# Kernel tuning notes

Hardware: AMD Instinct MI355X
Metric: run time of the kernel (lower is better)

## Reference

```python
import jax, jax.numpy as jnp
import numpy as np

LN_EPS = 1e-5

def _layernorm(x, gamma, beta):
    mu = jnp.mean(x, axis=-1, keepdims=True)
    var = jnp.mean(jnp.square(x - mu), axis=-1, keepdims=True)
    return (x - mu) * jax.lax.rsqrt(var + LN_EPS) * gamma + beta

def _gcn_layer(A_hat, H, W, b, g, beta):
    # batched dense-equivalent of per-batch torch.sparse.mm: (B,N,N)@(B,N,F)
    H = jnp.einsum('bnm,bmf->bnf', A_hat, H)
    H = H @ W + b            # Linear
    H = _layernorm(H, g, beta)
    return jax.nn.relu(H)    # dropout is identity in eval

def setup_inputs() -> dict:
    key = jax.random.key(0)
    ks = jax.random.split(key, 8)
    B, N, F, Hd, K, G = 16, 2048, 64, 256, 128, 18
    fuse = Hd + G  # 274
    return {
        'A_hat': jax.random.uniform(ks[0], (B, N, N), dtype=jnp.float32),
        'X': jax.random.normal(ks[1], (B, N, F), dtype=jnp.float32),
        'global_vec': jax.random.normal(ks[2], (B, G), dtype=jnp.float32),
        'W1': jax.random.normal(ks[3], (F, Hd), dtype=jnp.float32) / np.sqrt(F),
        'b1': jnp.zeros((Hd,), jnp.float32),
        'g1': jnp.ones((Hd,), jnp.float32),
        'beta1': jnp.zeros((Hd,), jnp.float32),
        'W2': jax.random.normal(ks[4], (Hd, Hd), dtype=jnp.float32) / np.sqrt(Hd),
        'b2': jnp.zeros((Hd,), jnp.float32),
        'g2': jnp.ones((Hd,), jnp.float32),
        'beta2': jnp.zeros((Hd,), jnp.float32),
        'Ws': jax.random.normal(ks[5], (fuse, 1), dtype=jnp.float32) / np.sqrt(fuse),
        'bs': jnp.zeros((1,), jnp.float32),
        'Wa': jax.random.normal(ks[6], (fuse, K), dtype=jnp.float32) / np.sqrt(fuse),
        'ba': jnp.zeros((K,), jnp.float32),
    }

def reference(A_hat, X, global_vec, W1, b1, g1, beta1, W2, b2, g2, beta2, Ws, bs, Wa, ba):
    H = _gcn_layer(A_hat, X, W1, b1, g1, beta1)
    H = _gcn_layer(A_hat, H, W2, b2, g2, beta2)
    gcnout = jnp.mean(H, axis=1)                       # 'mean' readout -> (B, hidden)
    fused = jnp.concatenate([gcnout, global_vec], axis=-1)  # (B, hidden+18)
    pred_y_reg = (fused @ Ws + bs)[:, 0]               # (B,)
    pred_arr_reg = fused @ Wa + ba                     # (B, K)
    return pred_y_reg, pred_arr_reg
```

## Files before the change

kernel.cpp:

```cpp
#include <hip/hip_runtime.h>

typedef unsigned short u16;
typedef __attribute__((ext_vector_type(8))) short bf16x8;
typedef __attribute__((ext_vector_type(16))) float f32x16;

__device__ __forceinline__ unsigned f2bf(float f) {
  unsigned u = __float_as_uint(f);
  return (u + 0x7fffu + ((u >> 16) & 1u)) >> 16;
}

__device__ __forceinline__ void async16(const u16* g, u16* l) {
  __builtin_amdgcn_global_load_lds(
      (const __attribute__((address_space(1))) void*)g,
      (__attribute__((address_space(3))) void*)l, 16, 0, 0);
}

__global__ __launch_bounds__(256) void prep(
    const float* __restrict__ A, u16* __restrict__ Abf,
    const float* __restrict__ X, u16* __restrict__ Xbf,
    const float* __restrict__ W1, u16* __restrict__ W1T,
    const float* __restrict__ W2, u16* __restrict__ W2T,
    float* __restrict__ GCN)
{
  const long long gid = (long long)blockIdx.x * 256 + threadIdx.x;
  const long long stride = (long long)gridDim.x * 256;
  for (long long i = gid; i < 8388608LL; i += stride) {
    const float4 a = ((const float4*)A)[2 * i];
    const float4 b = ((const float4*)A)[2 * i + 1];
    uint4 r;
    r.x = f2bf(a.x) | (f2bf(a.y) << 16);
    r.y = f2bf(a.z) | (f2bf(a.w) << 16);
    r.z = f2bf(b.x) | (f2bf(b.y) << 16);
    r.w = f2bf(b.z) | (f2bf(b.w) << 16);
    ((uint4*)Abf)[i] = r;
  }
  for (long long i = gid; i < 262144LL; i += stride) {
    const float4 a = ((const float4*)X)[2 * i];
    const float4 b = ((const float4*)X)[2 * i + 1];
    uint4 r;
    r.x = f2bf(a.x) | (f2bf(a.y) << 16);
    r.y = f2bf(a.z) | (f2bf(a.w) << 16);
    r.z = f2bf(b.x) | (f2bf(b.y) << 16);
    r.w = f2bf(b.z) | (f2bf(b.w) << 16);
    ((uint4*)Xbf)[i] = r;
  }
  for (long long i = gid; i < 16384LL; i += stride) {
    const int c = (int)(i >> 6), r = (int)(i & 63);
    W1T[i] = (u16)f2bf(W1[r * 256 + c]);
  }
  for (long long i = gid; i < 65536LL; i += stride) {
    const int c = (int)(i >> 8), r = (int)(i & 255);
    W2T[i] = (u16)f2bf(W2[r * 256 + c]);
  }
  if (gid < 4096) GCN[gid] = 0.f;
}

template<int EPI>
__global__ __launch_bounds__(512, 2) void mm128(
    const u16* __restrict__ Aop, const u16* __restrict__ Bop,
    int K, int lda, int ldb, int ldc,
    long long sA, long long sB, long long sC,
    const float* __restrict__ bias, const float* __restrict__ gam,
    const float* __restrict__ bet, u16* __restrict__ Cb, float* __restrict__ gcn)
{
  __shared__ __align__(16) u16 As[2][128 * 64];
  __shared__ __align__(16) u16 Bs[2][256 * 64];
  const int tid = threadIdx.x;
  const int w = tid >> 6, lane = tid & 63, l31 = lane & 31, half = lane >> 5;
  const int wm = w >> 2, wn = w & 3;

  const int fid = blockIdx.x + gridDim.x * (blockIdx.y + gridDim.y * blockIdx.z);
  const int pb = gridDim.x * gridDim.y;
  int idx = fid >> 3;
  int bz = fid & 7;
  if (idx >= pb) { bz += 8; idx -= pb; }
  const int m0 = (int)(idx % gridDim.x) * 128;
  const int n0 = (int)(idx / gridDim.x) * 256;

  const int srow = tid >> 3;
  const int clog = (tid & 7) ^ (srow & 7);
  const u16* Ag = Aop + sA * bz + (size_t)(m0 + srow) * lda + clog * 8;
  const u16* Bg = Bop + sB * bz + (size_t)(n0 + srow) * ldb + clog * 8;

  f32x16 acc[2][2];
#pragma unroll
  for (int i = 0; i < 2; i++)
#pragma unroll
    for (int j = 0; j < 2; j++)
#pragma unroll
      for (int r = 0; r < 16; r++) acc[i][j][r] = 0.f;

  const int niter = K >> 6;
  {
    u16* Ad = As[0]; u16* Bd = Bs[0];
    async16(Ag, Ad + tid * 8);
    async16(Ag + (size_t)64 * lda, Ad + 4096 + tid * 8);
#pragma unroll
    for (int p = 0; p < 4; p++)
      async16(Bg + (size_t)(p * 64) * ldb, Bd + p * 4096 + tid * 8);
  }

  for (int i = 0; i < niter; i++) {
    if (i + 1 < niter) {
      const int k1 = (i + 1) << 6;
      u16* Ad = As[(i + 1) & 1]; u16* Bd = Bs[(i + 1) & 1];
      async16(Ag + k1, Ad + tid * 8);
      async16(Ag + (size_t)64 * lda + k1, Ad + 4096 + tid * 8);
#pragma unroll
      for (int p = 0; p < 4; p++)
        async16(Bg + (size_t)(p * 64) * ldb + k1, Bd + p * 4096 + tid * 8);
      __builtin_amdgcn_s_waitcnt(0x0F76);
    } else {
      __builtin_amdgcn_s_waitcnt(0x0F70);
    }
    __builtin_amdgcn_s_barrier();
    __asm__ volatile("" ::: "memory");
    const u16* Ab = As[i & 1];
    const u16* Bb = Bs[i & 1];
#pragma unroll
    for (int kk = 0; kk < 4; kk++) {
      const int pc = ((kk * 2 + half) ^ (l31 & 7)) * 8;
      const bf16x8 a0 = *(const bf16x8*)(Ab + (wm * 64 + l31) * 64 + pc);
      const bf16x8 a1 = *(const bf16x8*)(Ab + (wm * 64 + 32 + l31) * 64 + pc);
      const bf16x8 b0 = *(const bf16x8*)(Bb + (wn * 64 + l31) * 64 + pc);
      const bf16x8 b1 = *(const bf16x8*)(Bb + (wn * 64 + 32 + l31) * 64 + pc);
      acc[0][0] = __builtin_amdgcn_mfma_f32_32x32x16_bf16(a0, b0, acc[0][0], 0, 0, 0);
      acc[0][1] = __builtin_amdgcn_mfma_f32_32x32x16_bf16(a0, b1, acc[0][1], 0, 0, 0);
      acc[1][0] = __builtin_amdgcn_mfma_f32_32x32x16_bf16(a1, b0, acc[1][0], 0, 0, 0);
      acc[1][1] = __builtin_amdgcn_mfma_f32_32x32x16_bf16(a1, b1, acc[1][1], 0, 0, 0);
    }
    __asm__ volatile("" ::: "memory");
    __builtin_amdgcn_s_barrier();
  }

  const int col0 = wn * 64 + l31;

  if constexpr (EPI == 0) {
#pragma unroll
    for (int mt = 0; mt < 2; mt++)
#pragma unroll
      for (int r = 0; r < 16; r++) {
        const int rl = (r & 3) + 8 * (r >> 2) + 4 * half;
        const long long row = (long long)m0 + wm * 64 + mt * 32 + rl;
        Cb[sC * bz + row * ldc + n0 + col0]      = (u16)f2bf(acc[mt][0][r]);
        Cb[sC * bz + row * ldc + n0 + col0 + 32] = (u16)f2bf(acc[mt][1][r]);
      }
    return;
  }

  __syncthreads();
  const float bia0 = bias[col0], bia1 = bias[col0 + 32];
  float s2[2][16];
#pragma unroll
  for (int mt = 0; mt < 2; mt++)
#pragma unroll
    for (int r = 0; r < 16; r++) {
      acc[mt][0][r] += bia0;
      acc[mt][1][r] += bia1;
      s2[mt][r] = acc[mt][0][r] + acc[mt][1][r];
    }
#pragma unroll
  for (int off = 1; off <= 16; off <<= 1)
#pragma unroll
    for (int mt = 0; mt < 2; mt++)
#pragma unroll
      for (int r = 0; r < 16; r++) s2[mt][r] += __shfl_xor(s2[mt][r], off);

  float* sm = (float*)As;
  if (l31 == 0) {
#pragma unroll
    for (int mt = 0; mt < 2; mt++)
#pragma unroll
      for (int r = 0; r < 16; r++) {
        const int rl = (r & 3) + 8 * (r >> 2) + 4 * half;
        sm[wn * 128 + wm * 64 + mt * 32 + rl] = s2[mt][r];
      }
  }
  __syncthreads();
  if (tid < 128)
    sm[512 + tid] = (sm[tid] + sm[128 + tid] + sm[256 + tid] + sm[384 + tid]) * (1.f / 256.f);
  __syncthreads();
  float4 mu4[2][4];
#pragma unroll
  for (int mt = 0; mt < 2; mt++)
#pragma unroll
    for (int g = 0; g < 4; g++)
      mu4[mt][g] = *(const float4*)(sm + 512 + wm * 64 + mt * 32 + g * 8 + 4 * half);

  float q2[2][16];
#pragma unroll
  for (int mt = 0; mt < 2; mt++)
#pragma unroll
    for (int r = 0; r < 16; r++) {
      const float mu = ((const float*)&mu4[mt][r >> 2])[r & 3];
      const float d0 = acc[mt][0][r] - mu, d1 = acc[mt][1][r] - mu;
      q2[mt][r] = d0 * d0 + d1 * d1;
    }
#pragma unroll
  for (int off = 1; off <= 16; off <<= 1)
#pragma unroll
    for (int mt = 0; mt < 2; mt++)
#pragma unroll
      for (int r = 0; r < 16; r++) q2[mt][r] += __shfl_xor(q2[mt][r], off);
  __syncthreads();
  if (l31 == 0) {
#pragma unroll
    for (int mt = 0; mt < 2; mt++)
#pragma unroll
      for (int r = 0; r < 16; r++) {
        const int rl = (r & 3) + 8 * (r >> 2) + 4 * half;
        sm[wn * 128 + wm * 64 + mt * 32 + rl] = q2[mt][r];
      }
  }
  __syncthreads();
  if (tid < 128)
    sm[640 + tid] = rsqrtf(
        (sm[tid] + sm[128 + tid] + sm[256 + tid] + sm[384 + tid]) * (1.f / 256.f) + 1e-5f);
  __syncthreads();
  float4 iv4[2][4];
#pragma unroll
  for (int mt = 0; mt < 2; mt++)
#pragma unroll
    for (int g = 0; g < 4; g++)
      iv4[mt][g] = *(const float4*)(sm + 640 + wm * 64 + mt * 32 + g * 8 + 4 * half);

  const float g0 = gam[col0], g1 = gam[col0 + 32];
  const float e0 = bet[col0], e1 = bet[col0 + 32];
  if constexpr (EPI == 1) {
#pragma unroll
    for (int mt = 0; mt < 2; mt++)
#pragma unroll
      for (int r = 0; r < 16; r++) {
        const float mu = ((const float*)&mu4[mt][r >> 2])[r & 3];
        const float iv = ((const float*)&iv4[mt][r >> 2])[r & 3];
        const int rl = (r & 3) + 8 * (r >> 2) + 4 * half;
        const long long row = (long long)m0 + wm * 64 + mt * 32 + rl;
        const float y0 = fmaxf((acc[mt][0][r] - mu) * iv * g0 + e0, 0.f);
        const float y1 = fmaxf((acc[mt][1][r] - mu) * iv * g1 + e1, 0.f);
        Cb[sC * bz + row * ldc + col0]      = (u16)f2bf(y0);
        Cb[sC * bz + row * ldc + col0 + 32] = (u16)f2bf(y1);
      }
  } else {
    float c0 = 0.f, c1 = 0.f;
#pragma unroll
    for (int mt = 0; mt < 2; mt++)
#pragma unroll
      for (int r = 0; r < 16; r++) {
        const float mu = ((const float*)&mu4[mt][r >> 2])[r & 3];
        const float iv = ((const float*)&iv4[mt][r >> 2])[r & 3];
        c0 += fmaxf((acc[mt][0][r] - mu) * iv * g0 + e0, 0.f);
        c1 += fmaxf((acc[mt][1][r] - mu) * iv * g1 + e1, 0.f);
      }
    c0 += __shfl_xor(c0, 32);
    c1 += __shfl_xor(c1, 32);
    if (half == 0) {
      atomicAdd(gcn + bz * 256 + col0, c0);
      atomicAdd(gcn + bz * 256 + col0 + 32, c1);
    }
  }
}

__global__ __launch_bounds__(128) void final_kernel(
    const float* __restrict__ gcn, const float* __restrict__ gv,
    const float* __restrict__ Ws, const float* __restrict__ bs,
    const float* __restrict__ Wa, const float* __restrict__ ba,
    float* __restrict__ out)
{
  const int b = blockIdx.x, t = threadIdx.x;
  __shared__ float fused[274];
  fused[t] = gcn[b * 256 + t] * (1.f / 2048.f);
  fused[128 + t] = gcn[b * 256 + 128 + t] * (1.f / 2048.f);
  if (t < 18) fused[256 + t] = gv[b * 18 + t];
  __syncthreads();
  float acc = ba[t];
  for (int i = 0; i < 274; i++) acc = fmaf(fused[i], Wa[i * 128 + t], acc);
  out[16 + b * 128 + t] = acc;
  if (t < 64) {
    float p = 0.f;
    for (int i = t; i < 274; i += 64) p += fused[i] * Ws[i];
#pragma unroll
    for (int off = 32; off >= 1; off >>= 1) p += __shfl_xor(p, off);
    if (t == 0) out[b] = p + bs[0];
  }
}

extern "C" void kernel_launch(void* const* d_in, const int* in_sizes, int n_in,
                              void* d_out, int out_size, void* d_ws, size_t ws_size,
                              hipStream_t stream)
{
  const float* A   = (const float*)d_in[0];
  const float* X   = (const float*)d_in[1];
  const float* GV  = (const float*)d_in[2];
  const float* W1  = (const float*)d_in[3];
  const float* b1  = (const float*)d_in[4];
  const float* g1  = (const float*)d_in[5];
  const float* be1 = (const float*)d_in[6];
  const float* W2  = (const float*)d_in[7];
  const float* b2  = (const float*)d_in[8];
  const float* g2  = (const float*)d_in[9];
  const float* be2 = (const float*)d_in[10];
  const float* Ws  = (const float*)d_in[11];
  const float* bs  = (const float*)d_in[12];
  const float* Wa  = (const float*)d_in[13];
  const float* ba  = (const float*)d_in[14];
  float* out = (float*)d_out;
  (void)in_sizes; (void)n_in; (void)out_size; (void)ws_size;

  char* ws = (char*)d_ws;
  u16*   Abf = (u16*)(ws + 0);
  u16*   Xbf = (u16*)(ws + 134217728);
  u16*   W1T = (u16*)(ws + 138412032);
  u16*   W2T = (u16*)(ws + 138444800);
  u16*   XWT = (u16*)(ws + 138575872);
  u16*   H1  = (u16*)(ws + 155353088);
  u16*   HWT = (u16*)(ws + 172130304);
  float* GCN = (float*)(ws + 188907520);

  prep<<<4096, 256, 0, stream>>>(A, Abf, X, Xbf, W1, W1T, W2, W2T, GCN);

  mm128<0><<<dim3(2, 8, 16), 512, 0, stream>>>(
      W1T, Xbf, 64, 64, 64, 2048, 0LL, 131072LL, 524288LL,
      nullptr, nullptr, nullptr, XWT, nullptr);

  mm128<1><<<dim3(16, 1, 16), 512, 0, stream>>>(
      Abf, XWT, 2048, 2048, 2048, 256, 4194304LL, 524288LL, 524288LL,
      b1, g1, be1, H1, nullptr);

  mm128<0><<<dim3(2, 8, 16), 512, 0, stream>>>(
      W2T, H1, 256, 256, 256, 2048, 0LL, 524288LL, 524288LL,
      nullptr, nullptr, nullptr, HWT, nullptr);

  mm128<2><<<dim3(16, 1, 16), 512, 0, stream>>>(
      Abf, HWT, 2048, 2048, 2048, 256, 4194304LL, 524288LL, 524288LL,
      b2, g2, be2, nullptr, GCN);

  final_kernel<<<16, 128, 0, stream>>>(GCN, GV, Ws, bs, Wa, ba, out);
}
```

Measured before the change: 599.7 us.

## Fuse H1·W2 transposed GEMM into first aggregation epilogue

Adds a new epilogue variant to the layer-1 aggregation GEMM. It keeps the LayerNorm+ReLU output tile (128 rows x 256 features) in LDS as bf16, then multiplies it by W2 streamed through double-buffered async loads and writes HWT directly. This removes one kernel launch and the global write and re-read of H1. In exchange, the aggregation kernel gets a longer tail with extra register pressure and barriers.

Result: no change. 592.2 us (-1.2%).

```diff
diff --git a/kernel.cpp b/kernel.cpp
--- a/kernel.cpp
+++ b/kernel.cpp
@@ -61,7 +61,8 @@
     int K, int lda, int ldb, int ldc,
     long long sA, long long sB, long long sC,
     const float* __restrict__ bias, const float* __restrict__ gam,
-    const float* __restrict__ bet, u16* __restrict__ Cb, float* __restrict__ gcn)
+    const float* __restrict__ bet, u16* __restrict__ Cb, float* __restrict__ gcn,
+    const u16* __restrict__ W2x)
 {
   __shared__ __align__(16) u16 As[2][128 * 64];
   __shared__ __align__(16) u16 Bs[2][256 * 64];
@@ -240,7 +241,7 @@
         Cb[sC * bz + row * ldc + col0]      = (u16)f2bf(y0);
         Cb[sC * bz + row * ldc + col0 + 32] = (u16)f2bf(y1);
       }
-  } else {
+  } else if constexpr (EPI == 2) {
     float c0 = 0.f, c1 = 0.f;
 #pragma unroll
     for (int mt = 0; mt < 2; mt++)
@@ -257,6 +258,85 @@
       atomicAdd(gcn + bz * 256 + col0, c0);
       atomicAdd(gcn + bz * 256 + col0 + 32, c1);
     }
+  } else {
+    char* H1loc = (char*)Bs;
+#pragma unroll
+    for (int mt = 0; mt < 2; mt++)
+#pragma unroll
+      for (int r = 0; r < 16; r++) {
+        const float mu = ((const float*)&mu4[mt][r >> 2])[r & 3];
+        const float iv = ((const float*)&iv4[mt][r >> 2])[r & 3];
+        const int rl = (r & 3) + 8 * (r >> 2) + 4 * half;
+        const int row = wm * 64 + mt * 32 + rl;
+        const float y0 = fmaxf((acc[mt][0][r] - mu) * iv * g0 + e0, 0.f);
+        const float y1 = fmaxf((acc[mt][1][r] - mu) * iv * g1 + e1, 0.f);
+        const int xo = (row & 31) << 4;
+        *(u16*)(H1loc + row * 512 + ((col0 * 2) ^ xo))        = (u16)f2bf(y0);
+        *(u16*)(H1loc + row * 512 + (((col0 + 32) * 2) ^ xo)) = (u16)f2bf(y1);
+      }
+    __syncthreads();
+
+    u16* Wc = (u16*)As;
+    const int orow = (w >> 1) * 64, mcol = (w & 1) * 64;
+    const int srw2 = tid >> 2;
+    const int cl2 = (tid & 3) ^ (srw2 & 3);
+
+    f32x16 a2[2][2];
+#pragma unroll
+    for (int i = 0; i < 2; i++)
+#pragma unroll
+      for (int j = 0; j < 2; j++)
+#pragma unroll
+        for (int r = 0; r < 16; r++) a2[i][j][r] = 0.f;
+
+#define STAGE_W2(c) do {                                                  \
+    u16* _d = Wc + ((c) & 1) * 8192 + tid * 8;                            \
+    const u16* _s = W2x + (size_t)srw2 * 256 + (c) * 32 + cl2 * 8;        \
+    async16(_s, _d);                                                      \
+    async16(_s + 128 * 256, _d + 4096);                                   \
+  } while (0)
+
+    STAGE_W2(0);
+    STAGE_W2(1);
+#pragma unroll
+    for (int c = 0; c < 8; c++) {
+      if (c < 7) __builtin_amdgcn_s_waitcnt(0x0F72);
+      else       __builtin_amdgcn_s_waitcnt(0x0F70);
+      __builtin_amdgcn_s_barrier();
+      __asm__ volatile("" ::: "memory");
+      const u16* bufc = Wc + (c & 1) * 8192;
+#pragma unroll
+      for (int kk = 0; kk < 2; kk++) {
+        const int sl = kk * 2 + half;
+        const int ao = (sl ^ (l31 & 3)) * 8;
+        const bf16x8 a0 = *(const bf16x8*)(bufc + (orow + l31) * 32 + ao);
+        const bf16x8 a1 = *(const bf16x8*)(bufc + (orow + 32 + l31) * 32 + ao);
+        const int kb = (c * 32 + sl * 8) * 2;
+        const int xo = l31 << 4;
+        const bf16x8 b0 = *(const bf16x8*)(H1loc + (mcol + l31) * 512 + (kb ^ xo));
+        const bf16x8 b1 = *(const bf16x8*)(H1loc + (mcol + 32 + l31) * 512 + (kb ^ xo));
+        a2[0][0] = __builtin_amdgcn_mfma_f32_32x32x16_bf16(a0, b0, a2[0][0], 0, 0, 0);
+        a2[0][1] = __builtin_amdgcn_mfma_f32_32x32x16_bf16(a0, b1, a2[0][1], 0, 0, 0);
+        a2[1][0] = __builtin_amdgcn_mfma_f32_32x32x16_bf16(a1, b0, a2[1][0], 0, 0, 0);
+        a2[1][1] = __builtin_amdgcn_mfma_f32_32x32x16_bf16(a1, b1, a2[1][1], 0, 0, 0);
+      }
+      __asm__ volatile("" ::: "memory");
+      __builtin_amdgcn_s_barrier();
+      if (c + 2 < 8) STAGE_W2(c + 2);
+    }
+#undef STAGE_W2
+
+#pragma unroll
+    for (int i = 0; i < 2; i++)
+#pragma unroll
+      for (int j = 0; j < 2; j++)
+#pragma unroll
+        for (int r = 0; r < 16; r++) {
+          const int rl = (r & 3) + 8 * (r >> 2) + 4 * half;
+          const long long rowo = orow + i * 32 + rl;
+          const long long colg = m0 + mcol + j * 32 + l31;
+          Cb[sC * bz + rowo * ldc + colg] = (u16)f2bf(a2[i][j][r]);
+        }
   }
 }
 
@@ -312,27 +392,22 @@
   u16*   W1T = (u16*)(ws + 138412032);
   u16*   W2T = (u16*)(ws + 138444800);
   u16*   XWT = (u16*)(ws + 138575872);
-  u16*   H1  = (u16*)(ws + 155353088);
-  u16*   HWT = (u16*)(ws + 172130304);
-  float* GCN = (float*)(ws + 188907520);
+  u16*   HWT = (u16*)(ws + 155353088);
+  float* GCN = (float*)(ws + 172130304);
 
   prep<<<4096, 256, 0, stream>>>(A, Abf, X, Xbf, W1, W1T, W2, W2T, GCN);
 
   mm128<0><<<dim3(2, 8, 16), 512, 0, stream>>>(
       W1T, Xbf, 64, 64, 64, 2048, 0LL, 131072LL, 524288LL,
-      nullptr, nullptr, nullptr, XWT, nullptr);
-
-  mm128<1><<<dim3(16, 1, 16), 512, 0, stream>>>(
-      Abf, XWT, 2048, 2048, 2048, 256, 4194304LL, 524288LL, 524288LL,
-      b1, g1, be1, H1, nullptr);
-
-  mm128<0><<<dim3(2, 8, 16), 512, 0, stream>>>(
-      W2T, H1, 256, 256, 256, 2048, 0LL, 524288LL, 524288LL,
-      nullptr, nullptr, nullptr, HWT, nullptr);
+      nullptr, nullptr, nullptr, XWT, nullptr, nullptr);
+
+  mm128<3><<<dim3(16, 1, 16), 512, 0, stream>>>(
+      Abf, XWT, 2048, 2048, 2048, 2048, 4194304LL, 524288LL, 524288LL,
+      b1, g1, be1, HWT, nullptr, W2T);
 
   mm128<2><<<dim3(16, 1, 16), 512, 0, stream>>>(
       Abf, HWT, 2048, 2048, 2048, 256, 4194304LL, 524288LL, 524288LL,
-      b2, g2, be2, nullptr, GCN);
+      b2, g2, be2, nullptr, GCN, nullptr);
 
   final_kernel<<<16, 128, 0, stream>>>(GCN, GV, Ws, bs, Wa, ba, out);
 }
```
